# Kernel optimization log

Hardware: AMD Instinct MI355X
Metric: run time of the kernel (lower is better)

## Reference

```python
import jax, jax.numpy as jnp
import numpy as np

# --- module hyperparameters (from init_kwargs) ---
NUM_CHANNELS = 31
WINDOW_SIZE = 3
IN_DIM = 2 * WINDOW_SIZE + 1          # 7
GRID_SIZE = 5
SPLINE_ORDER = 3
GRID_RANGE = (-1.0, 1.0)
N_BASIS = GRID_SIZE + SPLINE_ORDER    # 8 spline coefficients per input dim
COEF_LEN = IN_DIM * 1 * N_BASIS       # 56
KAN_PARAMS = COEF_LEN + IN_DIM + IN_DIM  # 70 = coef + univariate_w + residual_w


def bspline_basis(x):
    """Cox-de Boor B-spline bases of order SPLINE_ORDER on a uniform grid.
    x: [...,] -> returns [..., N_BASIS]."""
    lo, hi = GRID_RANGE
    h = (hi - lo) / GRID_SIZE
    # extended knot vector: grid_size + 2*k + 1 knots
    knots = lo + h * jnp.arange(-SPLINE_ORDER, GRID_SIZE + SPLINE_ORDER + 1,
                                dtype=x.dtype)
    xe = x[..., None]
    b = ((xe >= knots[:-1]) & (xe < knots[1:])).astype(x.dtype)
    for p in range(1, SPLINE_ORDER + 1):
        left = (xe - knots[: -(p + 1)]) / (knots[p:-1] - knots[: -(p + 1)]) * b[..., :-1]
        right = (knots[p + 1:] - xe) / (knots[p + 1:] - knots[1:-p]) * b[..., 1:]
        b = left + right
    return b  # [..., N_BASIS]


def setup_inputs() -> dict:
    key = jax.random.key(0)
    k1, k2, k3 = jax.random.split(key, 3)
    B, C, D, H, W = 2, NUM_CHANNELS, IN_DIM, 192, 192
    windowed_x = jax.random.normal(k1, (B, C, D, H, W), dtype=jnp.float32)
    # hypernetwork generator: 3x3 conv  C -> KAN_PARAMS
    gen_w = jax.random.normal(k2, (KAN_PARAMS, C, 3, 3), dtype=jnp.float32) * 0.05
    gen_b = jax.random.normal(k3, (KAN_PARAMS,), dtype=jnp.float32) * 0.05
    return {"windowed_x": windowed_x, "gen_w": gen_w, "gen_b": gen_b}


def reference(windowed_x, gen_w, gen_b):
    B, C, D, H, W = windowed_x.shape
    # shared-params branch: global context -> per-pixel KAN weights
    ctx = windowed_x.mean(axis=2)  # [B, C, H, W]
    wts = jax.lax.conv_general_dilated(
        ctx, gen_w, window_strides=(1, 1), padding="SAME",
        dimension_numbers=("NCHW", "OIHW", "NCHW"))
    wts = wts + gen_b[None, :, None, None]            # [B, P, H, W]
    wts = jnp.moveaxis(wts, 1, -1)                    # [B, H, W, P]
    # unpack per-pixel KAN parameters (out_dim == 1 squeezed)
    coef = wts[..., :COEF_LEN].reshape(B, H, W, D, N_BASIS)   # [B,H,W,7,8]
    uw = wts[..., COEF_LEN:COEF_LEN + D]                      # [B,H,W,7]
    rw = wts[..., COEF_LEN + D:COEF_LEN + 2 * D]              # [B,H,W,7]
    # per-pixel, per-channel spline window evaluation (weights shared over C)
    x = jnp.moveaxis(windowed_x, 2, -1)               # [B, C, H, W, 7]
    basis = bspline_basis(x)                          # [B, C, H, W, 7, 8]
    spline = jnp.einsum("bchwdg,bhwdg,bhwd->bchw", basis, coef, uw)
    resid = jnp.einsum("bchwd,bhwd->bchw", jax.nn.silu(x), rw)
    return spline + resid                             # [B, C, H, W]
```

## Files before the change

kernel.cpp:

```cpp
#include <hip/hip_runtime.h>
#include <math.h>

#define NBATCH 2
#define NC 31
#define ND 7
#define NH 192
#define NW 192
#define HW (NH * NW)
#define NP (NBATCH * HW)
#define NBASIS 8
#define CLEN 56
#define KP 70
#define OCB 5

#define CTSX 32
#define CTSY 32
#define WROWS 8
#define HROWS 10
#define HCOLS 34
#define WCELLS (HROWS * HCOLS)
#define NSLOT 6

#define KPX 64

__global__ __launch_bounds__(256) void ctx_mean_kernel(
    const float4* __restrict__ x4, float4* __restrict__ ctx4)
{
    const int HW4 = HW / 4;
    int idx = blockIdx.x * 256 + threadIdx.x;
    if (idx >= NBATCH * NC * HW4) return;
    int hw4 = idx % HW4;
    int bc  = idx / HW4;
    const float4* src = x4 + (size_t)bc * (ND * HW4) + hw4;
    float4 a = src[0];
#pragma unroll
    for (int d = 1; d < ND; ++d) {
        float4 v = src[d * HW4];
        a.x += v.x; a.y += v.y; a.z += v.z; a.w += v.w;
    }
    const float inv = 1.0f / 7.0f;
    a.x *= inv; a.y *= inv; a.z *= inv; a.w *= inv;
    ctx4[idx] = a;
}

__global__ __launch_bounds__(256, 4) void conv_kernel(
    const float* __restrict__ ctx, const float* __restrict__ gw,
    const float* __restrict__ gb, float* __restrict__ wts)
{
    __shared__ float tile[4][WCELLS];

    const int tid  = threadIdx.x;
    const int lane = tid & 63;
    const int wv   = tid >> 6;
    const int tx0  = blockIdx.x * CTSX;
    const int by   = blockIdx.y;
    const int b    = by / (NH / CTSY);
    const int ty0  = (by - b * (NH / CTSY)) * CTSY;
    const int oc0  = blockIdx.z * OCB;
    const int wrow0 = wv * WROWS;

    int   off[NSLOT];
    float msk[NSLOT];
    bool  stv[NSLOT];
#pragma unroll
    for (int s = 0; s < NSLOT; ++s) {
        int cell = lane + s * 64;
        int r = cell / HCOLS;
        int c = cell - r * HCOLS;
        int gh = ty0 + wrow0 + r - 1;
        int gc = tx0 + c - 1;
        bool ok = (gh >= 0) && (gh < NH) && (gc >= 0) && (gc < NW);
        int ghc = min(max(gh, 0), NH - 1);
        int gcc = min(max(gc, 0), NW - 1);
        off[s] = ghc * NW + gcc;
        msk[s] = ok ? 1.f : 0.f;
        stv[s] = (cell < WCELLS);
    }

    const float* cb  = ctx + (b * NC) * HW;
    float*       myt = tile[wv];

    {
        float t[NSLOT];
#pragma unroll
        for (int s = 0; s < NSLOT; ++s) t[s] = cb[off[s]] * msk[s];
#pragma unroll
        for (int s = 0; s < NSLOT; ++s)
            if (stv[s]) myt[lane + s * 64] = t[s];
    }

    float acc[OCB][4];
#pragma unroll
    for (int oc = 0; oc < OCB; ++oc) {
        float bv = gb[oc0 + oc];
#pragma unroll
        for (int k = 0; k < 4; ++k) acc[oc][k] = bv;
    }

    const int strip = lane >> 5;
    const int col   = lane & 31;
    const float* t0 = myt + (strip * 4) * HCOLS + col;

    for (int ic = 0; ic < NC; ++ic) {
        float nxt[NSLOT];
        if (ic + 1 < NC) {
            const float* src = cb + (ic + 1) * HW;
#pragma unroll
            for (int s = 0; s < NSLOT; ++s) nxt[s] = src[off[s]] * msk[s];
        }

        float v[6][3];
#pragma unroll
        for (int j = 0; j < 6; ++j)
#pragma unroll
            for (int c = 0; c < 3; ++c)
                v[j][c] = t0[j * HCOLS + c];

        const float* wb = gw + (oc0 * NC + ic) * 9;
#pragma unroll
        for (int oc = 0; oc < OCB; ++oc) {
            const float* w9 = wb + oc * (NC * 9);
            float w00 = w9[0], w01 = w9[1], w02 = w9[2];
            float w10 = w9[3], w11 = w9[4], w12 = w9[5];
            float w20 = w9[6], w21 = w9[7], w22 = w9[8];
#pragma unroll
            for (int k = 0; k < 4; ++k) {
                acc[oc][k] += v[k][0] * w00 + v[k][1] * w01 + v[k][2] * w02
                            + v[k + 1][0] * w10 + v[k + 1][1] * w11 + v[k + 1][2] * w12
                            + v[k + 2][0] * w20 + v[k + 2][1] * w21 + v[k + 2][2] * w22;
            }
        }

        if (ic + 1 < NC) {
#pragma unroll
            for (int s = 0; s < NSLOT; ++s)
                if (stv[s]) myt[lane + s * 64] = nxt[s];
        }
    }

    const int pbase = b * HW + (ty0 + wrow0 + strip * 4) * NW + (tx0 + col);
#pragma unroll
    for (int oc = 0; oc < OCB; ++oc)
#pragma unroll
        for (int k = 0; k < 4; ++k)
            wts[(oc0 + oc) * NP + pbase + k * NW] = acc[oc][k];
}

__device__ __forceinline__ float spline_part(float xv, const float* cb, int d)
{
    float t = __builtin_fmaf(xv, 2.5f, 5.5f);
    float fi = floorf(t);
    int i = (int)fi;
    float u = t - fi;
    float u2 = u * u, u3 = u2 * u;
    float um = 1.f - u;
    float w0 = um * um * um * (1.f / 6.f);
    float w3 = u3 * (1.f / 6.f);
    float w1 = (3.f * u3 - 6.f * u2 + 4.f) * (1.f / 6.f);
    float w2 = 1.f - w0 - w1 - w3;
    int j0 = i - 3;
    float sd = 0.f;
#pragma unroll
    for (int k = 0; k < 4; ++k) {
        int j = j0 + k;
        bool valid = ((unsigned)j) < 8u;
        int jc = j & 7;
        float wk = (k == 0) ? w0 : (k == 1) ? w1 : (k == 2) ? w2 : w3;
        float cf = cb[(d * NBASIS + jc) * KPX];
        sd += (valid ? wk : 0.f) * cf;
    }
    return sd;
}

__device__ __forceinline__ float silu(float xv)
{
    return xv / (1.f + __expf(-xv));
}

__global__ __launch_bounds__(256, 8) void kan_kernel(
    const float* __restrict__ x, const float* __restrict__ wts,
    float* __restrict__ out)
{
    __shared__ float scoef[KP * KPX];
    const int tid = threadIdx.x;
    const int p0  = blockIdx.x * KPX;

    for (int f = tid; f < KP * 32; f += 256) {
        int k = f >> 5;
        int g = f & 31;
        float2 v = *(const float2*)(wts + (size_t)k * NP + p0 + g * 2);
        *(float2*)(scoef + k * KPX + g * 2) = v;
    }
    __syncthreads();

    const int lane = tid & 63;
    const int wv   = tid >> 6;
    const int b    = p0 / HW;
    const int hw   = (p0 - b * HW) + lane;

    const float* cb = scoef + lane;

    float uw[ND], rw[ND];
#pragma unroll
    for (int d = 0; d < ND; ++d) {
        uw[d] = cb[(CLEN + d) * KPX];
        rw[d] = cb[(CLEN + ND + d) * KPX];
    }

    const int cy = blockIdx.y;
    const int c_begin = (cy == 0) ? wv * 4
                                  : ((wv == 3) ? 27 : 16 + wv * 4);

    const float* xb = x + (size_t)(b * NC) * (ND * HW) + hw;
    float* ob = out + (b * NC) * HW + hw;

    float acc[4] = {0.f, 0.f, 0.f, 0.f};
#pragma unroll
    for (int d = 0; d < ND; ++d) {
        float xv[4];
#pragma unroll
        for (int j = 0; j < 4; ++j)
            xv[j] = xb[((size_t)(c_begin + j) * ND + d) * HW];
#pragma unroll
        for (int j = 0; j < 4; ++j)
            acc[j] += uw[d] * spline_part(xv[j], cb, d) + rw[d] * silu(xv[j]);
    }
#pragma unroll
    for (int j = 0; j < 4; ++j)
        ob[(size_t)(c_begin + j) * HW] = acc[j];
}

extern "C" void kernel_launch(void* const* d_in, const int* in_sizes, int n_in,
                              void* d_out, int out_size, void* d_ws, size_t ws_size,
                              hipStream_t stream)
{
    const float* x  = (const float*)d_in[0];
    const float* gw = (const float*)d_in[1];
    const float* gb = (const float*)d_in[2];
    float* out = (float*)d_out;

    float* ctx = (float*)d_ws;
    float* wts = ctx + (size_t)NBATCH * NC * HW;

    int n4 = NBATCH * NC * (HW / 4);
    ctx_mean_kernel<<<dim3((n4 + 255) / 256), 256, 0, stream>>>(
        (const float4*)x, (float4*)ctx);
    conv_kernel<<<dim3(NW / CTSX, (NH / CTSY) * NBATCH, KP / OCB), 256, 0, stream>>>(ctx, gw, gb, wts);
    kan_kernel<<<dim3(NP / KPX, 2), 256, 0, stream>>>(x, wts, out);
}
```

Baseline: 165.5 us.

## Rewrite 3x3 hypernetwork conv as bf16 MFMA implicit GEMM

The scalar FP32 3x3 convolution is replaced with an implicit GEMM on MFMA 16x16x32 bf16 instructions. The mean kernel now also converts the generator weights to bf16 in a padded [tap][80 out][32 in] layout, staged in the output buffer as scratch. Each conv block handles 64 pixels of one row and stages a 3x66 halo of bf16 context channels in shared memory. This targets the FP32 ALU cost of the conv, but bf16 rounding of weights and activations reduces precision, and the LDS footprint per block is large.

```diff
diff --git a/kernel.cpp b/kernel.cpp
--- a/kernel.cpp
+++ b/kernel.cpp
@@ -11,139 +11,140 @@
 #define NBASIS 8
 #define CLEN 56
 #define KP 70
-#define OCB 5
-
-#define CTSX 32
-#define CTSY 32
-#define WROWS 8
-#define HROWS 10
-#define HCOLS 34
-#define WCELLS (HROWS * HCOLS)
-#define NSLOT 6
+
+#define N4 (NBATCH * NC * (HW / 4))
+#define GWB_N (9 * 80 * 32)
+
+#define A_WORDS (9 * 80 * 32)
+#define B_WORDS (3 * 66 * 32)
 
 #define KPX 64
 
+typedef __attribute__((ext_vector_type(8))) short s16x8;
+typedef __attribute__((ext_vector_type(4))) float f32x4;
+
+__device__ __forceinline__ unsigned short f2bf(float f)
+{
+    unsigned u = __float_as_uint(f);
+    u += 0x7FFFu + ((u >> 16) & 1u);
+    return (unsigned short)(u >> 16);
+}
+
 __global__ __launch_bounds__(256) void ctx_mean_kernel(
-    const float4* __restrict__ x4, float4* __restrict__ ctx4)
+    const float4* __restrict__ x4, float4* __restrict__ ctx4,
+    const float* __restrict__ gw, unsigned short* __restrict__ gwb)
 {
     const int HW4 = HW / 4;
     int idx = blockIdx.x * 256 + threadIdx.x;
-    if (idx >= NBATCH * NC * HW4) return;
-    int hw4 = idx % HW4;
-    int bc  = idx / HW4;
-    const float4* src = x4 + (size_t)bc * (ND * HW4) + hw4;
-    float4 a = src[0];
-#pragma unroll
-    for (int d = 1; d < ND; ++d) {
-        float4 v = src[d * HW4];
-        a.x += v.x; a.y += v.y; a.z += v.z; a.w += v.w;
-    }
-    const float inv = 1.0f / 7.0f;
-    a.x *= inv; a.y *= inv; a.z *= inv; a.w *= inv;
-    ctx4[idx] = a;
-}
-
-__global__ __launch_bounds__(256, 4) void conv_kernel(
-    const float* __restrict__ ctx, const float* __restrict__ gw,
+    if (idx < N4) {
+        int hw4 = idx % HW4;
+        int bc  = idx / HW4;
+        const float4* src = x4 + (size_t)bc * (ND * HW4) + hw4;
+        float4 a = src[0];
+#pragma unroll
+        for (int d = 1; d < ND; ++d) {
+            float4 v = src[d * HW4];
+            a.x += v.x; a.y += v.y; a.z += v.z; a.w += v.w;
+        }
+        const float inv = 1.0f / 7.0f;
+        a.x *= inv; a.y *= inv; a.z *= inv; a.w *= inv;
+        ctx4[idx] = a;
+        return;
+    }
+    int e = idx - N4;
+    if (e < GWB_N) {
+        int s  = e / 2560;
+        int r  = e - s * 2560;
+        int m  = r >> 5;
+        int ic = r & 31;
+        float v = (m < KP && ic < NC) ? gw[m * (NC * 9) + ic * 9 + s] : 0.f;
+        gwb[e] = f2bf(v);
+    }
+}
+
+__global__ __launch_bounds__(256) void conv_kernel(
+    const float* __restrict__ ctx, const unsigned short* __restrict__ gwb,
     const float* __restrict__ gb, float* __restrict__ wts)
 {
-    __shared__ float tile[4][WCELLS];
+    __shared__ __align__(16) unsigned short AB[A_WORDS + B_WORDS];
 
     const int tid  = threadIdx.x;
     const int lane = tid & 63;
     const int wv   = tid >> 6;
-    const int tx0  = blockIdx.x * CTSX;
-    const int by   = blockIdx.y;
-    const int b    = by / (NH / CTSY);
-    const int ty0  = (by - b * (NH / CTSY)) * CTSY;
-    const int oc0  = blockIdx.z * OCB;
-    const int wrow0 = wv * WROWS;
-
-    int   off[NSLOT];
-    float msk[NSLOT];
-    bool  stv[NSLOT];
-#pragma unroll
-    for (int s = 0; s < NSLOT; ++s) {
-        int cell = lane + s * 64;
-        int r = cell / HCOLS;
-        int c = cell - r * HCOLS;
-        int gh = ty0 + wrow0 + r - 1;
-        int gc = tx0 + c - 1;
-        bool ok = (gh >= 0) && (gh < NH) && (gc >= 0) && (gc < NW);
-        int ghc = min(max(gh, 0), NH - 1);
-        int gcc = min(max(gc, 0), NW - 1);
-        off[s] = ghc * NW + gcc;
-        msk[s] = ok ? 1.f : 0.f;
-        stv[s] = (cell < WCELLS);
-    }
-
-    const float* cb  = ctx + (b * NC) * HW;
-    float*       myt = tile[wv];
+    const int gr   = blockIdx.x / 3;
+    const int x0   = (blockIdx.x % 3) * 64;
+    const int b    = gr / NH;
+    const int y    = gr - b * NH;
 
     {
-        float t[NSLOT];
-#pragma unroll
-        for (int s = 0; s < NSLOT; ++s) t[s] = cb[off[s]] * msk[s];
-#pragma unroll
-        for (int s = 0; s < NSLOT; ++s)
-            if (stv[s]) myt[lane + s * 64] = t[s];
-    }
-
-    float acc[OCB][4];
-#pragma unroll
-    for (int oc = 0; oc < OCB; ++oc) {
-        float bv = gb[oc0 + oc];
-#pragma unroll
-        for (int k = 0; k < 4; ++k) acc[oc][k] = bv;
-    }
-
-    const int strip = lane >> 5;
-    const int col   = lane & 31;
-    const float* t0 = myt + (strip * 4) * HCOLS + col;
-
-    for (int ic = 0; ic < NC; ++ic) {
-        float nxt[NSLOT];
-        if (ic + 1 < NC) {
-            const float* src = cb + (ic + 1) * HW;
-#pragma unroll
-            for (int s = 0; s < NSLOT; ++s) nxt[s] = src[off[s]] * msk[s];
-        }
-
-        float v[6][3];
-#pragma unroll
-        for (int j = 0; j < 6; ++j)
-#pragma unroll
-            for (int c = 0; c < 3; ++c)
-                v[j][c] = t0[j * HCOLS + c];
-
-        const float* wb = gw + (oc0 * NC + ic) * 9;
-#pragma unroll
-        for (int oc = 0; oc < OCB; ++oc) {
-            const float* w9 = wb + oc * (NC * 9);
-            float w00 = w9[0], w01 = w9[1], w02 = w9[2];
-            float w10 = w9[3], w11 = w9[4], w12 = w9[5];
-            float w20 = w9[6], w21 = w9[7], w22 = w9[8];
-#pragma unroll
-            for (int k = 0; k < 4; ++k) {
-                acc[oc][k] += v[k][0] * w00 + v[k][1] * w01 + v[k][2] * w02
-                            + v[k + 1][0] * w10 + v[k + 1][1] * w11 + v[k + 1][2] * w12
-                            + v[k + 2][0] * w20 + v[k + 2][1] * w21 + v[k + 2][2] * w22;
+        const uint4* gs = (const uint4*)gwb;
+        uint4*       gd = (uint4*)AB;
+        for (int f = tid; f < A_WORDS / 8; f += 256) gd[f] = gs[f];
+    }
+
+    if (tid < 3 * 66) {
+        int row = tid / 66;
+        int col = tid - row * 66;
+        int gy = y + row - 1, gx = x0 + col - 1;
+        bool ok = (gy >= 0) && (gy < NH) && (gx >= 0) && (gx < NW);
+        int cgy = ok ? gy : 0, cgx = ok ? gx : 0;
+        const float* src = ctx + (size_t)(b * NC) * HW + cgy * NW + cgx;
+        unsigned dw[16];
+        if (ok) {
+            float v[NC];
+#pragma unroll
+            for (int ic = 0; ic < NC; ++ic) v[ic] = src[(size_t)ic * HW];
+#pragma unroll
+            for (int j = 0; j < 16; ++j) {
+                unsigned lo = f2bf(v[2 * j]);
+                unsigned hi = (2 * j + 1 < NC) ? (unsigned)f2bf(v[2 * j + 1]) : 0u;
+                dw[j] = lo | (hi << 16);
             }
-        }
-
-        if (ic + 1 < NC) {
-#pragma unroll
-            for (int s = 0; s < NSLOT; ++s)
-                if (stv[s]) myt[lane + s * 64] = nxt[s];
-        }
-    }
-
-    const int pbase = b * HW + (ty0 + wrow0 + strip * 4) * NW + (tx0 + col);
-#pragma unroll
-    for (int oc = 0; oc < OCB; ++oc)
-#pragma unroll
-        for (int k = 0; k < 4; ++k)
-            wts[(oc0 + oc) * NP + pbase + k * NW] = acc[oc][k];
+        } else {
+#pragma unroll
+            for (int j = 0; j < 16; ++j) dw[j] = 0u;
+        }
+        uint4* dst = (uint4*)(AB + A_WORDS + tid * 32);
+#pragma unroll
+        for (int q = 0; q < 4; ++q)
+            dst[q] = make_uint4(dw[4 * q], dw[4 * q + 1], dw[4 * q + 2], dw[4 * q + 3]);
+    }
+    __syncthreads();
+
+    const int lm = lane & 15;
+    const int kb = lane >> 4;
+
+    f32x4 acc[5];
+#pragma unroll
+    for (int mt = 0; mt < 5; ++mt)
+#pragma unroll
+        for (int j = 0; j < 4; ++j) {
+            int m = mt * 16 + kb * 4 + j;
+            acc[mt][j] = (m < KP) ? gb[m] : 0.f;
+        }
+
+    const unsigned short* ap = AB + lm * 32 + kb * 8;
+    const unsigned short* bp = AB + A_WORDS + (wv * 16 + lm) * 32 + kb * 8;
+
+#pragma unroll
+    for (int s = 0; s < 9; ++s) {
+        const int dy = s / 3, dx = s % 3;
+        s16x8 bf = *(const s16x8*)(bp + (dy * 66 + dx) * 32);
+#pragma unroll
+        for (int mt = 0; mt < 5; ++mt) {
+            s16x8 af = *(const s16x8*)(ap + (s * 80 + mt * 16) * 32);
+            acc[mt] = __builtin_amdgcn_mfma_f32_16x16x32_bf16(af, bf, acc[mt], 0, 0, 0);
+        }
+    }
+
+    const int p = blockIdx.x * 64 + wv * 16 + lm;
+#pragma unroll
+    for (int mt = 0; mt < 5; ++mt)
+#pragma unroll
+        for (int j = 0; j < 4; ++j) {
+            int m = mt * 16 + kb * 4 + j;
+            if (m < KP) wts[(size_t)m * NP + p] = acc[mt][j];
+        }
 }
 
 __device__ __forceinline__ float spline_part(float xv, const float* cb, int d)
@@ -241,10 +242,10 @@
 
     float* ctx = (float*)d_ws;
     float* wts = ctx + (size_t)NBATCH * NC * HW;
-
-    int n4 = NBATCH * NC * (HW / 4);
-    ctx_mean_kernel<<<dim3((n4 + 255) / 256), 256, 0, stream>>>(
-        (const float4*)x, (float4*)ctx);
-    conv_kernel<<<dim3(NW / CTSX, (NH / CTSY) * NBATCH, KP / OCB), 256, 0, stream>>>(ctx, gw, gb, wts);
+    unsigned short* gwb = (unsigned short*)d_out;
+
+    ctx_mean_kernel<<<dim3(N4 / 256 + (GWB_N + 255) / 256), 256, 0, stream>>>(
+        (const float4*)x, (float4*)ctx, gw, gwb);
+    conv_kernel<<<dim3(NP / 64), 256, 0, stream>>>(ctx, gwb, gb, wts);
     kan_kernel<<<dim3(NP / KPX, 2), 256, 0, stream>>>(x, wts, out);
 }
```

New measurement: 142.7 us. 1.16x faster.
